# Optimization experiments

Measured on AMD Instinct MI355X. Metric: run time of the kernel, lower is better.

Reference implementation:

```python
import jax, jax.numpy as jnp
import numpy as np

B, F, HU, HC = 8192, 100, 128, 512


def _lin(key, din, dout, bias=True, scale=0.02):
    k1, k2 = jax.random.split(key)
    w = jax.random.normal(k1, (din, dout), jnp.float32) * scale
    if bias:
        b = jax.random.normal(k2, (dout,), jnp.float32) * scale
        return w, b
    return (w,)


def setup_inputs() -> dict:
    key = jax.random.key(0)
    ks = jax.random.split(key, 24)
    d = {}
    d['feature_list'] = jax.random.normal(ks[0], (B, F), jnp.float32)
    d['is_treat'] = jax.random.uniform(ks[1], (B,), jnp.float32)
    d['emb'] = jax.random.normal(ks[2], (F, HU), jnp.float32) * 0.02
    d['t_w'], d['t_b'] = _lin(ks[3], 1, HU)
    d['qw'], d['qb'] = _lin(ks[4], HU, HU)
    d['kw'], d['kb'] = _lin(ks[5], HU, HU)
    d['vw'], d['vb'] = _lin(ks[6], HU, HU)
    (d['a1w'],) = _lin(ks[7], HU, HU, bias=False)
    d['a2w'], d['a2b'] = _lin(ks[8], HU, HU)
    (d['a3w'],) = _lin(ks[9], HU, 1, bias=False)
    d['c1w'], d['c1b'] = _lin(ks[10], F * HU, HC)
    d['c2w'], d['c2b'] = _lin(ks[11], HC, HC)
    d['c3w'], d['c3b'] = _lin(ks[12], HC, HC // 2)
    d['c4w'], d['c4b'] = _lin(ks[13], HC // 2, HC // 4)
    d['c5w'], d['c5b'] = _lin(ks[14], HC // 4, HC // 8)
    d['clw'], d['clb'] = _lin(ks[15], HC // 8, 1)
    d['ctw'], d['ctb'] = _lin(ks[16], HC // 8, 1)
    d['u1w'], d['u1b'] = _lin(ks[17], HU, HU)
    d['u2w'], d['u2b'] = _lin(ks[18], HU, HU // 2)
    d['u3w'], d['u3b'] = _lin(ks[19], HU // 2, HU // 4)
    d['u4w'], d['u4b'] = _lin(ks[20], HU // 4, HU // 8)
    d['tlw'], d['tlb'] = _lin(ks[21], HU // 8, 1)
    d['utw'], d['utb'] = _lin(ks[22], HU // 8, 1)
    return d


def reference(feature_list, is_treat, emb, t_w, t_b, qw, qb, kw, kb, vw, vb,
              a1w, a2w, a2b, a3w, c1w, c1b, c2w, c2b, c3w, c3b, c4w, c4b,
              c5w, c5b, clw, clb, ctw, ctb, u1w, u1b, u2w, u2b, u3w, u3b,
              u4w, u4b, tlw, tlb, utw, utb):
    elu = jax.nn.elu
    sig = jax.nn.sigmoid
    b, f = feature_list.shape
    h = emb.shape[1]
    # per-feature embedding: [B, F, H]
    x_rep = feature_list[:, :, None] * emb[None, :, :]
    # normalize over the feature axis (dim=1), as in torch.linalg.norm(dim=1)
    nx = x_rep / jnp.linalg.norm(x_rep, axis=1, keepdims=True)
    # self-attention with sigmoid-then-softmax scores
    Q = nx @ qw + qb
    K = nx @ kw + kb
    V = nx @ vw + vb
    scores = jnp.einsum('bfh,bgh->bfg', Q, K) / (h ** 0.5)
    attn_w = jax.nn.softmax(sig(scores), axis=-1)
    xx = jnp.einsum('bfg,bgh->bfh', attn_w, V).reshape(b, f * h)
    # control net tower
    c = elu(xx @ c1w + c1b)
    c = elu(c @ c2w + c2b)
    c = elu(c @ c3w + c3b)
    c = elu(c @ c4w + c4b)
    c = elu(c @ c5w + c5b)  # is_self=True
    c_logit = c @ clw + clb
    c_tau = c @ ctw + ctb
    c_prob = sig(c_logit)
    # treatment representation: Linear(1, hu) on ones -> [B, H]
    t_rep = jnp.ones((b, 1), feature_list.dtype) @ t_w.reshape(1, h) + t_b
    # interaction attention (vectorized over features)
    att = jax.nn.relu(sig(t_rep @ a1w)[:, None, :] + sig(x_rep @ a2w + a2b))
    att = (att @ a3w)[..., 0]  # [B, F]
    attn = jax.nn.softmax(att, axis=1)
    xt = jnp.einsum('bf,bfh->bh', attn, x_rep)
    # uplift net tower
    u = elu(xt @ u1w + u1b)
    u = elu(u @ u2w + u2b)
    u = elu(u @ u3w + u3b)
    u = elu(u @ u4w + u4b)  # is_self=True
    t_logit = u @ tlw + tlb
    u_tau = u @ utw + utb
    t_prob = sig(t_logit)
    return (c_logit, c_prob, c_tau, t_logit, t_prob, u_tau)
```

## Files before the change

### kernel.cpp

```cpp
#include <hip/hip_runtime.h>
#include <hip/hip_bf16.h>

typedef __bf16 bf16;
typedef __bf16 bf16x8 __attribute__((ext_vector_type(8)));
typedef __bf16 bf16x4 __attribute__((ext_vector_type(4)));
typedef float f32x4 __attribute__((ext_vector_type(4)));
typedef unsigned u32x4 __attribute__((ext_vector_type(4)));

#define DEVI static __device__ __forceinline__

DEVI float sigmoidf_(float x){ return 1.0f/(1.0f+__expf(-x)); }
DEVI float eluf_(float x){ return x>0.f ? x : (__expf(x)-1.f); }
DEVI f32x4 mfma16(bf16x8 a, bf16x8 b, f32x4 c){ return __builtin_amdgcn_mfma_f32_16x16x32_bf16(a,b,c,0,0,0); }
DEVI f32x4 mfma8(long a, long b, f32x4 c){ return __builtin_amdgcn_mfma_f32_16x16x32_fp8_fp8(a,b,c,0,0,0); }
DEVI unsigned pack2_(float a, float b){
    union { bf16 v[2]; unsigned u; } t; t.v[0]=(bf16)a; t.v[1]=(bf16)b; return t.u;
}
DEVI unsigned long long pack4_(float a, float b, float c, float d){
    union { bf16 v[4]; unsigned long long u; } t;
    t.v[0]=(bf16)a; t.v[1]=(bf16)b; t.v[2]=(bf16)c; t.v[3]=(bf16)d; return t.u;
}
DEVI unsigned cvtfp8x4_(float a, float b, float c, float d){
    int v = __builtin_amdgcn_cvt_pk_fp8_f32(a, b, 0, false);
    v = __builtin_amdgcn_cvt_pk_fp8_f32(c, d, v, true);
    return (unsigned)v;
}
DEVI bf16x8 ldb64x2(const bf16* p0, const bf16* p1){
    union { bf16x8 v8; bf16x4 v4[2]; } u;
    u.v4[0] = *(const bf16x4*)p0;
    u.v4[1] = *(const bf16x4*)p1;
    return u.v8;
}

#define B_ 8192
#define F_ 100
#define FP 112
#define H_ 128
#define KC_ 12800
#define SPLIT_ 4
#define FP8SC 16.0f

#define SWZ(r,bc) ((bc) ^ (((r)&7)<<4))

DEVI void dotrans_(float (*t)[33], const float* in, bf16* out, int R, int C, int bx, int by, int tid){
    int c0 = bx*32, r0 = by*32;
    int tc = tid & 31, tr = tid >> 5;
    #pragma unroll
    for (int i=0;i<4;i++){
        int r = tr + i*8;
        t[r][tc] = in[(size_t)(r0+r)*C + c0 + tc];
    }
    __syncthreads();
    #pragma unroll
    for (int i=0;i<4;i++){
        int ro = tr + i*8;
        out[(size_t)(c0+ro)*R + r0 + tc] = (bf16)t[tc][ro];
    }
}

__global__ void k_prep_all(const float* __restrict__ qw, const float* __restrict__ qb,
                           const float* __restrict__ kw, const float* __restrict__ kb,
                           const float* __restrict__ tw, const float* __restrict__ tb,
                           const float* __restrict__ a1w, const float* __restrict__ vw,
                           const float* __restrict__ a2w, const float* __restrict__ c2w,
                           const float* __restrict__ c3w,
                           bf16* __restrict__ mextT, float* __restrict__ sigt, float* __restrict__ cconst,
                           bf16* __restrict__ wvT, bf16* __restrict__ wa2t,
                           bf16* __restrict__ c2wt, bf16* __restrict__ c3wt){
    __shared__ float t[32][33];
    const float rsc = 0.08838834764831845f;
    int blk = blockIdx.x, tid = threadIdx.x;
    if (blk < 9){
        #pragma unroll 1
        for (int e=0; e<8; ++e){
            int idx = e*256 + tid;
            int n = blk*16 + (idx>>7), h = idx&127;
            float acc = 0.f;
            if (n < 128){
                for (int d=0; d<128; ++d) acc += qw[h*128+d]*kw[n*128+d];
            } else if (n == 128){
                for (int d=0; d<128; ++d) acc += qw[h*128+d]*kb[d];
            } else if (n == 129){
                for (int d=0; d<128; ++d) acc += kw[h*128+d]*qb[d];
            }
            mextT[n*128+h] = (bf16)(acc*rsc);
        }
    } else if (blk == 9){
        if (tid < 128){
            float acc = 0.f;
            for (int h=0; h<128; ++h) acc += (tw[h]+tb[h]) * a1w[h*128+tid];
            sigt[tid] = sigmoidf_(acc);
        } else if (tid == 128){
            float acc = 0.f;
            for (int d=0; d<128; ++d) acc += qb[d]*kb[d];
            cconst[0] = acc*rsc;
        }
    } else if (blk < 26){
        int i = blk-10; dotrans_(t, vw, wvT, 128,128, i&3, i>>2, tid);
    } else if (blk < 42){
        int i = blk-26; dotrans_(t, a2w, wa2t, 128,128, i&3, i>>2, tid);
    } else if (blk < 298){
        int i = blk-42; dotrans_(t, c2w, c2wt, 512,512, i&15, i>>4, tid);
    } else {
        int i = blk-298; dotrans_(t, c3w, c3wt, 512,256, i&7, i>>3, tid);
    }
}

DEVI int kappa_(int k){
    int f = k>>7, h = k&127;
    if (f < 96)
        return (((f>>4)<<3) | (h>>4))*256 + ((f&15)>>2)*64 + (h&15)*4 + (f&3);
    else
        return 12288 + (h>>4)*64 + (h&15)*4 + (f&3);
}
__global__ void k_tc_kappa8(const float* __restrict__ in, unsigned char* __restrict__ out){
    __shared__ float t[32][33];
    const int C = 512;
    int c0 = blockIdx.x*32, r0 = blockIdx.y*32;
    int tc = threadIdx.x & 31, tr = threadIdx.x >> 5;
    #pragma unroll
    for (int i=0;i<4;i++){
        int r = tr + i*8;
        t[r][tc] = in[(size_t)(r0+r)*C + c0 + tc];
    }
    __syncthreads();
    #pragma unroll
    for (int i=0;i<4;i++){
        int ro = tr + i*8;
        float x = t[tc][ro]*FP8SC;
        int v = __builtin_amdgcn_cvt_pk_fp8_f32(x, x, 0, false);
        out[(size_t)(c0+ro)*KC_ + kappa_(r0+tc)] = (unsigned char)v;
    }
}

__global__ __launch_bounds__(256,2) void k_gatt(
    const float* __restrict__ feat, const float* __restrict__ emb,
    const bf16* __restrict__ wa2t, const float* __restrict__ a2b,
    const float* __restrict__ a3w, const float* __restrict__ sigt,
    float* __restrict__ attg)
{
    __shared__ bf16 sAt[128][72];
    __shared__ bf16 sBt[128][72];
    __shared__ float sRed[2][128];
    int tid=threadIdx.x, w=tid>>6, lane=tid&63, l15=lane&15, l4=lane>>4;
    int m0 = blockIdx.x*128;
    int wr = w>>1, wc = w&1;
    f32x4 acc[4][4];
    #pragma unroll
    for(int mi=0;mi<4;mi++)
        #pragma unroll
        for(int ni=0;ni<4;ni++) acc[mi][ni] = (f32x4){0.f,0.f,0.f,0.f};

    #pragma unroll 1
    for (int k0=0; k0<128; k0+=64){
        __syncthreads();
        #pragma unroll
        for (int t4=0; t4<4; t4++){
            int t = tid + t4*256;
            int row=t>>3, col=(t&7)*8;
            int gr = m0+row;
            int bb = gr/112, ff = gr - bb*112;
            bf16x8 o;
            if (ff < F_){
                float fv = feat[(size_t)bb*F_ + ff];
                const float* ep = emb + ff*H_ + k0 + col;
                f32x4 e0 = *(const f32x4*)ep;
                f32x4 e1 = *(const f32x4*)(ep+4);
                o[0]=(bf16)(fv*e0[0]); o[1]=(bf16)(fv*e0[1]); o[2]=(bf16)(fv*e0[2]); o[3]=(bf16)(fv*e0[3]);
                o[4]=(bf16)(fv*e1[0]); o[5]=(bf16)(fv*e1[1]); o[6]=(bf16)(fv*e1[2]); o[7]=(bf16)(fv*e1[3]);
            } else {
                #pragma unroll
                for (int e=0;e<8;e++) o[e]=(bf16)0.f;
            }
            *(bf16x8*)&sAt[row][col] = o;
            *(bf16x8*)&sBt[row][col] = *(const bf16x8*)(wa2t + row*H_ + k0 + col);
        }
        __syncthreads();
        #pragma unroll
        for(int ks=0;ks<2;ks++){
            bf16x8 af[4], bfr[4];
            #pragma unroll
            for(int mi=0;mi<4;mi++) af[mi] = *(const bf16x8*)&sAt[wr*64+mi*16+l15][ks*32+l4*8];
            #pragma unroll
            for(int ni=0;ni<4;ni++) bfr[ni] = *(const bf16x8*)&sBt[wc*64+ni*16+l15][ks*32+l4*8];
            #pragma unroll
            for(int mi=0;mi<4;mi++)
                #pragma unroll
                for(int ni=0;ni<4;ni++)
                    acc[mi][ni] = mfma16(af[mi], bfr[ni], acc[mi][ni]);
        }
    }
    float sg[4], ab[4], a3[4];
    #pragma unroll
    for (int ni=0;ni<4;ni++){
        int n = wc*64 + ni*16 + l15;
        sg[ni]=sigt[n]; ab[ni]=a2b[n]; a3[ni]=a3w[n];
    }
    #pragma unroll
    for (int mi=0;mi<4;mi++){
        float sj[4] = {0.f,0.f,0.f,0.f};
        #pragma unroll
        for (int ni=0;ni<4;ni++){
            #pragma unroll
            for (int j=0;j<4;j++){
                float u = sigmoidf_(acc[mi][ni][j] + ab[ni]);
                float t = sg[ni] + u;
                t = t>0.f ? t : 0.f;
                sj[j] += t*a3[ni];
            }
        }
        #pragma unroll
        for (int j=0;j<4;j++){
            float v = sj[j];
            #pragma unroll
            for (int m=1;m<16;m<<=1) v += __shfl_xor(v,m,16);
            sj[j]=v;
        }
        if (l15==0){
            #pragma unroll
            for (int j=0;j<4;j++) sRed[wc][wr*64+mi*16+l4*4+j] = sj[j];
        }
    }
    __syncthreads();
    if (tid < 128) attg[(size_t)m0 + tid] = sRed[0][tid] + sRed[1][tid];
}

__global__ __launch_bounds__(512,2) void k_attn2(
    const float* __restrict__ feat, const float* __restrict__ emb,
    const bf16* __restrict__ mextT, const bf16* __restrict__ wvT,
    const float* __restrict__ vb, const float* __restrict__ cconst,
    const float* __restrict__ attg,
    unsigned char* __restrict__ xxb, bf16* __restrict__ xtb)
{
    __shared__ char L[81792];
    char* Lm = L;
    char* Ln = L + 33280;
    float* sFeat  = (float*)(L+61952);
    float* sAw    = (float*)(L+62400);
    float* normP  = (float*)(L+62848);
    float* xtP    = (float*)(L+66944);
    float* sNorm  = (float*)(L+80384);
    float* sAlpha = (float*)(L+80896);
    float* sBeta  = (float*)(L+81344);

    int b = blockIdx.x;
    int tid = threadIdx.x, w = tid>>6, lane = tid&63;
    int l15 = lane&15, l4 = lane>>4;
    bf16 (*sP)[72] = (bf16(*)[72])(L + 61952 + w*2304);

    bf16x8 awv[4];
    #pragma unroll
    for (int kc=0;kc<4;kc++)
        awv[kc] = *(const bf16x8*)(wvT + (w*16+l15)*H_ + kc*32 + l4*8);
    float vbr[4];
    #pragma unroll
    for (int j=0;j<4;j++) vbr[j] = vb[w*16+l4*4+j];

    #pragma unroll 2
    for (int v = tid; v < 130*16; v += 512){
        int n = v >> 4, cg = (v & 15) * 8;
        *(u32x4*)(Lm + n*256 + SWZ(n, cg*2)) = *(const u32x4*)(mextT + n*128 + cg);
    }
    if (tid < FP) sFeat[tid] = (tid<F_) ? feat[(size_t)b*F_+tid] : 0.f;
    if (w==0){
        const float* ag = attg + (size_t)b*FP;
        float a0 = (lane<F_)? ag[lane] : -1e30f;
        float a1 = (lane+64<F_)? ag[lane+64] : -1e30f;
        float m = fmaxf(a0,a1);
        #pragma unroll
        for(int s=1;s<64;s<<=1) m = fmaxf(m, __shfl_xor(m,s,64));
        float e0 = (lane<F_)? __expf(a0-m):0.f;
        float e1 = (lane+64<F_)? __expf(a1-m):0.f;
        float s = e0+e1;
        #pragma unroll
        for(int t=1;t<64;t<<=1) s += __shfl_xor(s,t,64);
        float inv = 1.f/s;
        if (lane<FP) sAw[lane] = e0*inv;
        if (lane+64<FP) sAw[lane+64] = e1*inv;
    }
    __syncthreads();

    int hp = (tid&63)*2, gg = tid>>6;
    {
        float fa0=0.f, fa1=0.f;
        #pragma unroll 4
        for (int it=0; it<13; ++it){
            int f = gg + 8*it;
            if (f < F_){
                float2 e2 = *(const float2*)(emb + f*H_ + hp);
                float v0 = sFeat[f]*e2.x, v1 = sFeat[f]*e2.y;
                fa0 += v0*v0; fa1 += v1*v1;
            }
        }
        *(float2*)(normP + gg*128 + hp) = make_float2(fa0, fa1);
    }
    __syncthreads();
    if (tid < 128){
        float s = 0.f;
        #pragma unroll
        for (int g2=0; g2<8; ++g2) s += normP[g2*128 + tid];
        sNorm[tid] = sqrtf(s);
    }
    __syncthreads();

    {
        float rn0 = __builtin_amdgcn_rcpf(sNorm[hp]);
        float rn1 = __builtin_amdgcn_rcpf(sNorm[hp+1]);
        #pragma unroll 4
        for (int it=0; it<13; ++it){
            int f = gg + 8*it;
            if (f < F_){
                float2 e2 = *(const float2*)(emb + f*H_ + hp);
                *(unsigned*)(Ln + f*256 + SWZ(f, hp*2)) = pack2_(sFeat[f]*e2.x*rn0, sFeat[f]*e2.y*rn1);
            }
        }
        for (int z=tid; z<768; z+=512){
            int f = 100 + (z>>6), hz = (z&63)*2;
            *(unsigned*)(Ln + f*256 + SWZ(f, hz*2)) = 0u;
        }
    }
    __syncthreads();

    int mt = w;

    if (mt < 7){
        int nrow = 128 + (l15&1);
        bf16x8 bfr8[4];
        #pragma unroll
        for (int kc=0;kc<4;kc++)
            bfr8[kc] = *(const bf16x8*)(Lm + nrow*256 + SWZ(nrow, (kc*32+l4*8)*2));
        f32x4 acc = {0.f,0.f,0.f,0.f};
        #pragma unroll
        for (int kc=0;kc<4;kc++){
            bf16x8 a = *(const bf16x8*)(Ln + (mt*16+l15)*256 + SWZ(mt*16+l15, (kc*32+l4*8)*2));
            acc = mfma16(a, bfr8[kc], acc);
        }
        if (l15==0){
            #pragma unroll
            for (int j=0;j<4;j++) sAlpha[mt*16+l4*4+j] = acc[j];
        }
        if (l15==1){
            #pragma unroll
            for (int j=0;j<4;j++) sBeta[mt*16+l4*4+j] = acc[j];
        }
    }
    {
        int g4 = tid>>7, h = tid&127;
        float acc=0.f;
        #pragma unroll 5
        for (int it=0; it<25; ++it){
            int f = g4 + 4*it;
            acc += sAw[f] * (float)*(const bf16*)(Ln + f*256 + SWZ(f, h*2));
        }
        xtP[g4*128+h] = acc;
    }
    __syncthreads();
    if (tid < 128)
        xtb[(size_t)b*H_+tid] = (bf16)((xtP[tid]+xtP[128+tid]+xtP[256+tid]+xtP[384+tid]) * sNorm[tid]);
    __syncthreads();

    const float cc = cconst[0];
    unsigned uexB[3][2];
    float inv_[4];
    if (mt < 7){
        bf16x8 afxi[4];
        #pragma unroll
        for (int kc=0;kc<4;kc++)
            afxi[kc] = *(const bf16x8*)(Ln + (mt*16+l15)*256 + SWZ(mt*16+l15, (kc*32+l4*8)*2));
        f32x4 sc[7];
        #pragma unroll
        for (int gt=0; gt<7; gt++) sc[gt] = (f32x4){0.f,0.f,0.f,0.f};
        #pragma unroll 1
        for (int p=0; p<2; p++){
            #pragma unroll 2
            for (int nt4=0; nt4<4; nt4++){
                int nt = p*4 + nt4;
                bf16x8 bw[4];
                #pragma unroll
                for (int kc=0;kc<4;kc++)
                    bw[kc] = *(const bf16x8*)(Lm + (nt*16+l15)*256 + SWZ(nt*16+l15, (kc*32+l4*8)*2));
                f32x4 d = {0.f,0.f,0.f,0.f};
                #pragma unroll
                for (int kc=0;kc<4;kc++) d = mfma16(afxi[kc], bw[kc], d);
                #pragma unroll
                for (int j=0;j<4;j++) sP[l4*4+j][nt4*16+l15] = (bf16)d[j];
            }
            bf16x8 afs0 = *(const bf16x8*)&sP[l15][l4*8];
            bf16x8 afs1 = *(const bf16x8*)&sP[l15][32+l4*8];
            #pragma unroll
            for (int gt=0; gt<7; gt++){
                int r = gt*16+l15;
                bf16x8 b0 = *(const bf16x8*)(Ln + r*256 + SWZ(r, (p*64 + l4*8)*2));
                bf16x8 b1 = *(const bf16x8*)(Ln + r*256 + SWZ(r, (p*64 + 32 + l4*8)*2));
                sc[gt] = mfma16(afs0, b0, sc[gt]);
                sc[gt] = mfma16(afs1, b1, sc[gt]);
            }
        }
        float aj[4];
        #pragma unroll
        for (int j=0;j<4;j++) aj[j] = sAlpha[mt*16+l4*4+j];
        float rs[4] = {0.f,0.f,0.f,0.f};
        #pragma unroll
        for (int gt=0; gt<7; gt++){
            float bg = sBeta[gt*16+l15];
            int g = gt*16+l15;
            float e[4];
            #pragma unroll
            for (int j=0;j<4;j++){
                float val = sc[gt][j] + aj[j] + bg + cc;
                e[j] = (g<F_) ? __expf(sigmoidf_(val)) : 0.f;
                rs[j] += e[j];
            }
            if (gt < 4){
                #pragma unroll
                for (int j=0;j<4;j++) sP[l4*4+j][gt*16+l15] = (bf16)e[j];
            } else {
                uexB[gt-4][0] = pack2_(e[0],e[1]);
                uexB[gt-4][1] = pack2_(e[2],e[3]);
            }
        }
        #pragma unroll
        for (int j=0;j<4;j++){
            float v = rs[j];
            #pragma unroll
            for (int m2=1;m2<16;m2<<=1) v += __shfl_xor(v,m2,16);
            inv_[j] = 1.f/v;
        }
    }

    unsigned vpk[7][2];
    {
        #pragma unroll
        for (int gt=0; gt<7; gt++){
            f32x4 acc = {0.f,0.f,0.f,0.f};
            #pragma unroll
            for (int kc=0;kc<4;kc++){
                int r = gt*16+l15;
                bf16x8 bfr = *(const bf16x8*)(Ln + r*256 + SWZ(r, (kc*32+l4*8)*2));
                acc = mfma16(awv[kc], bfr, acc);
            }
            vpk[gt][0] = pack2_(acc[0]+vbr[0], acc[1]+vbr[1]);
            vpk[gt][1] = pack2_(acc[2]+vbr[2], acc[3]+vbr[3]);
        }
    }
    __syncthreads();

    union UP { unsigned u; bf16 v[2]; };
    {
        int ht = w;
        #pragma unroll
        for (int gt=0; gt<7; gt++){
            UP u0, u1;
            u0.u = vpk[gt][0]; u1.u = vpk[gt][1];
            int r0 = ht*16+l4*4;
            *(bf16*)(Ln + (r0  )*224 + SWZ(r0,   (gt*16+l15)*2)) = u0.v[0];
            *(bf16*)(Ln + (r0+1)*224 + SWZ(r0+1, (gt*16+l15)*2)) = u0.v[1];
            *(bf16*)(Ln + (r0+2)*224 + SWZ(r0+2, (gt*16+l15)*2)) = u1.v[0];
            *(bf16*)(Ln + (r0+3)*224 + SWZ(r0+3, (gt*16+l15)*2)) = u1.v[1];
        }
    }
    __syncthreads();

    if (mt < 7){
        bf16x8 ap0 = *(const bf16x8*)&sP[l15][l4*8];
        bf16x8 ap1 = *(const bf16x8*)&sP[l15][32+l4*8];
        f32x4 acc8[8];
        #pragma unroll
        for (int ht=0;ht<8;ht++) acc8[ht] = (f32x4){0.f,0.f,0.f,0.f};
        #pragma unroll
        for (int ht=0; ht<8; ht++){
            int r = ht*16+l15;
            int c0 = l4*8, c1 = 32+l4*8;
            acc8[ht] = mfma16(ap0, ldb64x2((const bf16*)(Ln + r*224 + SWZ(r, c0*2)),
                                           (const bf16*)(Ln + r*224 + SWZ(r, (c0+4)*2))), acc8[ht]);
            acc8[ht] = mfma16(ap1, ldb64x2((const bf16*)(Ln + r*224 + SWZ(r, c1*2)),
                                           (const bf16*)(Ln + r*224 + SWZ(r, (c1+4)*2))), acc8[ht]);
        }
        #pragma unroll
        for (int gt=4; gt<7; gt++){
            #pragma unroll
            for (int j2=0; j2<2; j2++){
                UP u; u.u = uexB[gt-4][j2];
                sP[l4*4+j2*2  ][(gt-4)*16+l15] = u.v[0];
                sP[l4*4+j2*2+1][(gt-4)*16+l15] = u.v[1];
            }
        }
        #pragma unroll
        for (int j=0;j<4;j++) sP[l4*4+j][48+l15] = (bf16)0.f;
        bf16x8 ap2 = *(const bf16x8*)&sP[l15][l4*8];
        bf16x8 ap3 = *(const bf16x8*)&sP[l15][32+l4*8];
        #pragma unroll
        for (int ht=0; ht<8; ht++){
            int r = ht*16+l15;
            int c2 = 64+l4*8;
            int c3 = 96+l4*8;  if (c3 >= 112) c3 = 96;
            acc8[ht] = mfma16(ap2, ldb64x2((const bf16*)(Ln + r*224 + SWZ(r, c2*2)),
                                           (const bf16*)(Ln + r*224 + SWZ(r, (c2+4)*2))), acc8[ht]);
            acc8[ht] = mfma16(ap3, ldb64x2((const bf16*)(Ln + r*224 + SWZ(r, c3*2)),
                                           (const bf16*)(Ln + r*224 + SWZ(r, (c3+4)*2))), acc8[ht]);
        }
        float fs[4];
        #pragma unroll
        for (int j=0;j<4;j++) fs[j] = inv_[j]*FP8SC;
        #pragma unroll
        for (int ht=0; ht<8; ht++){
            unsigned u = cvtfp8x4_(acc8[ht][0]*fs[0], acc8[ht][1]*fs[1], acc8[ht][2]*fs[2], acc8[ht][3]*fs[3]);
            if (mt < 6){
                *(unsigned*)(xxb + (size_t)b*KC_ + (mt*8+ht)*256 + lane*4) = u;
            } else if (l4 == 0){
                *(unsigned*)(xxb + (size_t)b*KC_ + 12288 + ht*64 + l15*4) = u;
            }
        }
    }
}

__global__ __launch_bounds__(256,2) void k_gemm_fp8(const unsigned char* __restrict__ A,
        const unsigned char* __restrict__ Bt, float* __restrict__ part, int M, int N, int K, int KS)
{
    __shared__ unsigned char sA[128][72];
    __shared__ unsigned char sB[128][72];
    int tid=threadIdx.x, w=tid>>6, lane=tid&63, l15=lane&15, l4=lane>>4;
    int m0 = blockIdx.y*128, n0 = blockIdx.x*128;
    int kbeg = blockIdx.z*KS, kend = kbeg + KS;
    int wr = w>>1, wc = w&1;
    f32x4 acc[4][4];
    #pragma unroll
    for(int mi=0;mi<4;mi++)
        #pragma unroll
        for(int ni=0;ni<4;ni++) acc[mi][ni] = (f32x4){0.f,0.f,0.f,0.f};

    for (int k0=kbeg; k0<kend; k0+=64){
        __syncthreads();
        #pragma unroll
        for (int t2=0;t2<2;t2++){
            int t = tid + t2*256;
            int row=t>>2, col=(t&3)*16;
            *(u32x4*)&sA[row][col] = *(const u32x4*)(A + (size_t)(m0+row)*K + k0 + col);
            *(u32x4*)&sB[row][col] = *(const u32x4*)(Bt + (size_t)(n0+row)*K + k0 + col);
        }
        __syncthreads();
        #pragma unroll
        for(int ks=0;ks<2;ks++){
            long af[4], bfr[4];
            #pragma unroll
            for(int mi=0;mi<4;mi++) af[mi] = *(const long*)&sA[wr*64+mi*16+l15][ks*32+l4*8];
            #pragma unroll
            for(int ni=0;ni<4;ni++) bfr[ni] = *(const long*)&sB[wc*64+ni*16+l15][ks*32+l4*8];
            #pragma unroll
            for(int mi=0;mi<4;mi++)
                #pragma unroll
                for(int ni=0;ni<4;ni++)
                    acc[mi][ni] = mfma8(af[mi], bfr[ni], acc[mi][ni]);
        }
    }
    float* pz = part + (size_t)blockIdx.z*M*N;
    #pragma unroll
    for(int mi=0;mi<4;mi++)
        #pragma unroll
        for(int ni=0;ni<4;ni++){
            int col = n0 + wc*64 + ni*16 + l15;
            #pragma unroll
            for(int j=0;j<4;j++){
                int row = m0 + wr*64 + mi*16 + l4*4 + j;
                pz[(size_t)row*N + col] = acc[mi][ni][j];
            }
        }
}

__global__ void k_c1fin(const float* __restrict__ part, const float* __restrict__ bias,
                        bf16* __restrict__ out){
    const size_t MN = (size_t)B_*512;
    size_t e0 = ((size_t)blockIdx.x*256 + threadIdx.x)*4;
    f32x4 s = *(const f32x4*)(part + e0);
    s += *(const f32x4*)(part + MN + e0);
    s += *(const f32x4*)(part + 2*MN + e0);
    s += *(const f32x4*)(part + 3*MN + e0);
    f32x4 bb = *(const f32x4*)(bias + (e0 & 511));
    const float ds = 1.0f/(FP8SC*FP8SC);
    unsigned long long u = pack4_(eluf_(s[0]*ds+bb[0]), eluf_(s[1]*ds+bb[1]),
                                  eluf_(s[2]*ds+bb[2]), eluf_(s[3]*ds+bb[3]));
    *(unsigned long long*)(out + e0) = u;
}

template<int BN, bool ELU>
__global__ __launch_bounds__(256,2) void k_gemm(const bf16* __restrict__ A, const bf16* __restrict__ Bt,
        const float* __restrict__ bias, bf16* __restrict__ out, int M, int N, int K)
{
    __shared__ bf16 sAt[128][72];
    __shared__ bf16 sBt[BN][72];
    int tid=threadIdx.x, w=tid>>6, lane=tid&63, l15=lane&15, l4=lane>>4;
    int m0 = blockIdx.y*128, n0 = blockIdx.x*BN;
    constexpr int MI = (BN==128)?4:2;
    constexpr int NI = (BN==128)?4:BN/16;
    int wr = (BN==128)? (w>>1) : w;
    int wc = (BN==128)? (w&1) : 0;
    f32x4 acc[MI][NI];
    #pragma unroll
    for(int mi=0;mi<MI;mi++)
        #pragma unroll
        for(int ni=0;ni<NI;ni++) acc[mi][ni] = (f32x4){0.f,0.f,0.f,0.f};

    for (int k0=0; k0<K; k0+=64){
        __syncthreads();
        for (int t=tid; t<128*8; t+=256){
            int row=t>>3, col=(t&7)*8;
            *(bf16x8*)&sAt[row][col] = *(const bf16x8*)(A + (size_t)(m0+row)*K + k0 + col);
        }
        for (int t=tid; t<BN*8; t+=256){
            int row=t>>3, col=(t&7)*8;
            *(bf16x8*)&sBt[row][col] = *(const bf16x8*)(Bt + (size_t)(n0+row)*K + k0 + col);
        }
        __syncthreads();
        #pragma unroll
        for(int ks=0;ks<2;ks++){
            bf16x8 af[MI], bfr[NI];
            #pragma unroll
            for(int mi=0;mi<MI;mi++) af[mi] = *(const bf16x8*)&sAt[wr*(MI*16)+mi*16+l15][ks*32+l4*8];
            #pragma unroll
            for(int ni=0;ni<NI;ni++) bfr[ni] = *(const bf16x8*)&sBt[wc*64+ni*16+l15][ks*32+l4*8];
            #pragma unroll
            for(int mi=0;mi<MI;mi++)
                #pragma unroll
                for(int ni=0;ni<NI;ni++)
                    acc[mi][ni] = mfma16(af[mi], bfr[ni], acc[mi][ni]);
        }
    }
    #pragma unroll
    for(int mi=0;mi<MI;mi++)
        #pragma unroll
        for(int ni=0;ni<NI;ni++){
            int col = n0 + wc*64 + ni*16 + l15;
            float bc = bias[col];
            #pragma unroll
            for(int j=0;j<4;j++){
                int row = m0 + wr*(MI*16) + mi*16 + l4*4 + j;
                float v = acc[mi][ni][j] + bc;
                if (ELU) v = eluf_(v);
                out[(size_t)row*N + col] = (bf16)v;
            }
        }
}

__global__ __launch_bounds__(256,2) void k_ctail(const bf16* __restrict__ c3o,
    const float* __restrict__ c4w, const float* __restrict__ c4b,
    const float* __restrict__ c5w, const float* __restrict__ c5b,
    const float* __restrict__ clw, const float* __restrict__ clb,
    const float* __restrict__ ctw, const float* __restrict__ ctb, float* __restrict__ outp)
{
    __shared__ float sA[32][260];
    __shared__ float sB[32][132];
    __shared__ float sC[32][68];
    int tid = threadIdx.x; int r0 = blockIdx.x*32;
    for (int v=tid; v<32*64; v+=256){
        int r=v>>6, c=(v&63)*4;
        bf16x4 x = *(const bf16x4*)(c3o + (size_t)(r0+r)*256 + c);
        sA[r][c]=(float)x[0]; sA[r][c+1]=(float)x[1]; sA[r][c+2]=(float)x[2]; sA[r][c+3]=(float)x[3];
    }
    __syncthreads();
    {
        int j = tid&127, rb = tid>>7;
        float acc[16];
        #pragma unroll
        for (int i=0;i<16;i++) acc[i]=c4b[j];
        #pragma unroll 4
        for (int h=0;h<256;h++){
            float wv = c4w[h*128+j];
            #pragma unroll
            for (int i=0;i<16;i++) acc[i] += sA[2*i+rb][h]*wv;
        }
        #pragma unroll
        for (int i=0;i<16;i++) sB[2*i+rb][j] = eluf_(acc[i]);
    }
    __syncthreads();
    {
        int j = tid&63, rb = tid>>6;
        float acc[8];
        #pragma unroll
        for (int i=0;i<8;i++) acc[i]=c5b[j];
        #pragma unroll 4
        for (int h=0;h<128;h++){
            float wv = c5w[h*64+j];
            #pragma unroll
            for (int i=0;i<8;i++) acc[i] += sB[4*i+rb][h]*wv;
        }
        #pragma unroll
        for (int i=0;i<8;i++) sC[4*i+rb][j] = eluf_(acc[i]);
    }
    __syncthreads();
    if (tid < 32){
        float r1 = clb[0], r2 = ctb[0];
        #pragma unroll 8
        for (int k=0;k<64;k++){ float v = sC[tid][k]; r1 += v*clw[k]; r2 += v*ctw[k]; }
        int row = r0 + tid;
        outp[row] = r1;
        outp[B_ + row] = sigmoidf_(r1);
        outp[(size_t)2*B_ + row] = r2;
    }
}

__global__ __launch_bounds__(256,2) void k_utower(const bf16* __restrict__ xtb,
    const float* __restrict__ u1w, const float* __restrict__ u1b,
    const float* __restrict__ u2w, const float* __restrict__ u2b,
    const float* __restrict__ u3w, const float* __restrict__ u3b,
    const float* __restrict__ u4w, const float* __restrict__ u4b,
    const float* __restrict__ tlw, const float* __restrict__ tlb,
    const float* __restrict__ utw, const float* __restrict__ utb, float* __restrict__ outp)
{
    __shared__ float sA[32][132];
    __shared__ float sB[32][132];
    __shared__ float sC[32][68];
    __shared__ float sD[32][36];
    __shared__ float sE[32][20];
    int tid = threadIdx.x; int r0 = blockIdx.x*32;
    for (int v=tid; v<32*32; v+=256){
        int r=v>>5, c=(v&31)*4;
        bf16x4 x = *(const bf16x4*)(xtb + (size_t)(r0+r)*128 + c);
        sA[r][c]=(float)x[0]; sA[r][c+1]=(float)x[1]; sA[r][c+2]=(float)x[2]; sA[r][c+3]=(float)x[3];
    }
    __syncthreads();
    {
        int j = tid&127, rb = tid>>7;
        float acc[16];
        #pragma unroll
        for (int i=0;i<16;i++) acc[i]=u1b[j];
        #pragma unroll 4
        for (int h=0;h<128;h++){
            float wv = u1w[h*128+j];
            #pragma unroll
            for (int i=0;i<16;i++) acc[i] += sA[2*i+rb][h]*wv;
        }
        #pragma unroll
        for (int i=0;i<16;i++) sB[2*i+rb][j] = eluf_(acc[i]);
    }
    __syncthreads();
    {
        int j = tid&63, rb = tid>>6;
        float acc[8];
        #pragma unroll
        for (int i=0;i<8;i++) acc[i]=u2b[j];
        #pragma unroll 4
        for (int h=0;h<128;h++){
            float wv = u2w[h*64+j];
            #pragma unroll
            for (int i=0;i<8;i++) acc[i] += sB[4*i+rb][h]*wv;
        }
        #pragma unroll
        for (int i=0;i<8;i++) sC[4*i+rb][j] = eluf_(acc[i]);
    }
    __syncthreads();
    {
        int j = tid&31, rb = tid>>5;
        float acc[4];
        #pragma unroll
        for (int i=0;i<4;i++) acc[i]=u3b[j];
        #pragma unroll 4
        for (int h=0;h<64;h++){
            float wv = u3w[h*32+j];
            #pragma unroll
            for (int i=0;i<4;i++) acc[i] += sC[8*i+rb][h]*wv;
        }
        #pragma unroll
        for (int i=0;i<4;i++) sD[8*i+rb][j] = eluf_(acc[i]);
    }
    __syncthreads();
    {
        int j = tid&15, rb = tid>>4;
        float acc[2];
        acc[0]=u4b[j]; acc[1]=u4b[j];
        #pragma unroll 4
        for (int h=0;h<32;h++){
            float wv = u4w[h*16+j];
            acc[0] += sD[rb][h]*wv;
            acc[1] += sD[16+rb][h]*wv;
        }
        sE[rb][j] = eluf_(acc[0]);
        sE[16+rb][j] = eluf_(acc[1]);
    }
    __syncthreads();
    if (tid < 32){
        float r1 = tlb[0], r2 = utb[0];
        #pragma unroll
        for (int k=0;k<16;k++){ float v = sE[tid][k]; r1 += v*tlw[k]; r2 += v*utw[k]; }
        int row = r0 + tid;
        outp[(size_t)3*B_ + row] = r1;
        outp[(size_t)4*B_ + row] = sigmoidf_(r1);
        outp[(size_t)5*B_ + row] = r2;
    }
}

extern "C" void kernel_launch(void* const* d_in, const int* in_sizes, int n_in,
                              void* d_out, int out_size, void* d_ws, size_t ws_size,
                              hipStream_t stream) {
    const float* feat=(const float*)d_in[0];
    const float* emb =(const float*)d_in[2];
    const float* t_w =(const float*)d_in[3]; const float* t_b=(const float*)d_in[4];
    const float* qw  =(const float*)d_in[5]; const float* qb =(const float*)d_in[6];
    const float* kw  =(const float*)d_in[7]; const float* kb =(const float*)d_in[8];
    const float* vw  =(const float*)d_in[9]; const float* vb =(const float*)d_in[10];
    const float* a1w =(const float*)d_in[11];
    const float* a2w =(const float*)d_in[12]; const float* a2b=(const float*)d_in[13];
    const float* a3w =(const float*)d_in[14];
    const float* c1w =(const float*)d_in[15]; const float* c1b=(const float*)d_in[16];
    const float* c2w =(const float*)d_in[17]; const float* c2b=(const float*)d_in[18];
    const float* c3w =(const float*)d_in[19]; const float* c3b=(const float*)d_in[20];
    const float* c4w =(const float*)d_in[21]; const float* c4b=(const float*)d_in[22];
    const float* c5w =(const float*)d_in[23]; const float* c5b=(const float*)d_in[24];
    const float* clw =(const float*)d_in[25]; const float* clb=(const float*)d_in[26];
    const float* ctw =(const float*)d_in[27]; const float* ctb=(const float*)d_in[28];
    const float* u1w =(const float*)d_in[29]; const float* u1b=(const float*)d_in[30];
    const float* u2w =(const float*)d_in[31]; const float* u2b=(const float*)d_in[32];
    const float* u3w =(const float*)d_in[33]; const float* u3b=(const float*)d_in[34];
    const float* u4w =(const float*)d_in[35]; const float* u4b=(const float*)d_in[36];
    const float* tlw =(const float*)d_in[37]; const float* tlb=(const float*)d_in[38];
    const float* utw =(const float*)d_in[39]; const float* utb=(const float*)d_in[40];
    float* outp = (float*)d_out;

    char* ws = (char*)d_ws;
    size_t off = 0;
    auto alloc = [&](size_t bytes)->char*{ char* p = ws + off; off += (bytes + 255) & ~(size_t)255; return p; };
    unsigned char* xxb = (unsigned char*)alloc((size_t)B_*KC_);
    float* part  = (float*)alloc((size_t)SPLIT_*B_*512*4);
    float* attg  = (float*)alloc((size_t)B_*FP*4);
    bf16* xtb    = (bf16*)alloc((size_t)B_*128*2);
    bf16* cbuf1  = (bf16*)alloc((size_t)B_*512*2);
    bf16* mextT  = (bf16*)alloc(144*128*2);
    bf16* wvT    = (bf16*)alloc(128*128*2);
    bf16* wa2t   = (bf16*)alloc(128*128*2);
    unsigned char* c1wtk8 = (unsigned char*)alloc((size_t)512*KC_);
    bf16* c2wt   = (bf16*)alloc((size_t)512*512*2);
    bf16* c3wt   = (bf16*)alloc((size_t)512*256*2);
    float* sigt  = (float*)alloc(128*4);
    float* cconst= (float*)alloc(4);
    bf16* cbuf2 = (bf16*)(xxb);
    bf16* cbuf3 = (bf16*)(xxb + (16u<<20));
    (void)ws_size; (void)in_sizes; (void)n_in; (void)out_size;

    k_prep_all<<<426,256,0,stream>>>(qw,qb,kw,kb,t_w,t_b,a1w, vw, a2w, c2w, c3w,
                                     mextT, sigt, cconst, wvT, wa2t, c2wt, c3wt);
    k_tc_kappa8<<<dim3(16,400),256,0,stream>>>(c1w, c1wtk8);

    k_gatt<<<7168,256,0,stream>>>(feat, emb, wa2t, a2b, a3w, sigt, attg);

    k_attn2<<<B_,512,0,stream>>>(feat,emb,mextT,wvT,vb,cconst,attg, xxb, xtb);

    k_utower<<<256,256,0,stream>>>(xtb,u1w,u1b,u2w,u2b,u3w,u3b,u4w,u4b,tlw,tlb,utw,utb,outp);

    k_gemm_fp8<<<dim3(4,64,SPLIT_),256,0,stream>>>(xxb, c1wtk8, part, B_,512,KC_, KC_/SPLIT_);
    k_c1fin<<<4096,256,0,stream>>>(part, c1b, cbuf1);

    k_gemm<128,true><<<dim3(4,64),256,0,stream>>>(cbuf1, c2wt, c2b, cbuf2, B_,512,512);
    k_gemm<128,true><<<dim3(2,64),256,0,stream>>>(cbuf2, c3wt, c3b, cbuf3, B_,256,512);
    k_ctail<<<256,256,0,stream>>>(cbuf3,c4w,c4b,c5w,c5b,clw,clb,ctw,ctb,outp);
}
```

Measured before the change: 728.2 us.

## Reduce c1 split-K, single-pass gatt staging, transposed MFMA layouts in attn2

Halves the split-K factor for the big fp8 c1 GEMM, which cuts partial-sum traffic and the reduction work in the finalize kernel, at the cost of fewer blocks and longer K loops per block. The gatt kernel now stages the full 128-wide K dimension in shared memory in one pass instead of two, removing a barrier round. The attention kernel swaps MFMA operand order so outputs land row-contiguous, which allows packed 64-bit shared-memory stores and drops scalar bf16 scatter and shuffle reductions. The V tile is written into the freed Lm buffer with full 16-byte reads, and the softmax inverse is passed through shared memory.

```diff
diff --git a/kernel.cpp b/kernel.cpp
--- a/kernel.cpp
+++ b/kernel.cpp
@@ -25,19 +25,13 @@
     v = __builtin_amdgcn_cvt_pk_fp8_f32(c, d, v, true);
     return (unsigned)v;
 }
-DEVI bf16x8 ldb64x2(const bf16* p0, const bf16* p1){
-    union { bf16x8 v8; bf16x4 v4[2]; } u;
-    u.v4[0] = *(const bf16x4*)p0;
-    u.v4[1] = *(const bf16x4*)p1;
-    return u.v8;
-}
 
 #define B_ 8192
 #define F_ 100
 #define FP 112
 #define H_ 128
 #define KC_ 12800
-#define SPLIT_ 4
+#define SPLIT_ 2
 #define FP8SC 16.0f
 
 #define SWZ(r,bc) ((bc) ^ (((r)&7)<<4))
@@ -139,8 +133,8 @@
     const float* __restrict__ a3w, const float* __restrict__ sigt,
     float* __restrict__ attg)
 {
-    __shared__ bf16 sAt[128][72];
-    __shared__ bf16 sBt[128][72];
+    __shared__ bf16 sAt[128][136];
+    __shared__ bf16 sBt[128][136];
     __shared__ float sRed[2][128];
     int tid=threadIdx.x, w=tid>>6, lane=tid&63, l15=lane&15, l4=lane>>4;
     int m0 = blockIdx.x*128;
@@ -151,44 +145,40 @@
         #pragma unroll
         for(int ni=0;ni<4;ni++) acc[mi][ni] = (f32x4){0.f,0.f,0.f,0.f};
 
-    #pragma unroll 1
-    for (int k0=0; k0<128; k0+=64){
-        __syncthreads();
-        #pragma unroll
-        for (int t4=0; t4<4; t4++){
-            int t = tid + t4*256;
-            int row=t>>3, col=(t&7)*8;
-            int gr = m0+row;
-            int bb = gr/112, ff = gr - bb*112;
-            bf16x8 o;
-            if (ff < F_){
-                float fv = feat[(size_t)bb*F_ + ff];
-                const float* ep = emb + ff*H_ + k0 + col;
-                f32x4 e0 = *(const f32x4*)ep;
-                f32x4 e1 = *(const f32x4*)(ep+4);
-                o[0]=(bf16)(fv*e0[0]); o[1]=(bf16)(fv*e0[1]); o[2]=(bf16)(fv*e0[2]); o[3]=(bf16)(fv*e0[3]);
-                o[4]=(bf16)(fv*e1[0]); o[5]=(bf16)(fv*e1[1]); o[6]=(bf16)(fv*e1[2]); o[7]=(bf16)(fv*e1[3]);
-            } else {
-                #pragma unroll
-                for (int e=0;e<8;e++) o[e]=(bf16)0.f;
-            }
-            *(bf16x8*)&sAt[row][col] = o;
-            *(bf16x8*)&sBt[row][col] = *(const bf16x8*)(wa2t + row*H_ + k0 + col);
-        }
-        __syncthreads();
-        #pragma unroll
-        for(int ks=0;ks<2;ks++){
-            bf16x8 af[4], bfr[4];
-            #pragma unroll
-            for(int mi=0;mi<4;mi++) af[mi] = *(const bf16x8*)&sAt[wr*64+mi*16+l15][ks*32+l4*8];
-            #pragma unroll
-            for(int ni=0;ni<4;ni++) bfr[ni] = *(const bf16x8*)&sBt[wc*64+ni*16+l15][ks*32+l4*8];
-            #pragma unroll
-            for(int mi=0;mi<4;mi++)
-                #pragma unroll
-                for(int ni=0;ni<4;ni++)
-                    acc[mi][ni] = mfma16(af[mi], bfr[ni], acc[mi][ni]);
-        }
+    #pragma unroll 2
+    for (int t8=0; t8<8; t8++){
+        int v = tid + t8*256;
+        int row = v>>4, colg = (v&15)*8;
+        int gr = m0+row;
+        int bb = gr/112, ff = gr - bb*112;
+        bf16x8 o;
+        if (ff < F_){
+            float fv = feat[(size_t)bb*F_ + ff];
+            const float* ep = emb + ff*H_ + colg;
+            f32x4 e0 = *(const f32x4*)ep;
+            f32x4 e1 = *(const f32x4*)(ep+4);
+            o[0]=(bf16)(fv*e0[0]); o[1]=(bf16)(fv*e0[1]); o[2]=(bf16)(fv*e0[2]); o[3]=(bf16)(fv*e0[3]);
+            o[4]=(bf16)(fv*e1[0]); o[5]=(bf16)(fv*e1[1]); o[6]=(bf16)(fv*e1[2]); o[7]=(bf16)(fv*e1[3]);
+        } else {
+            #pragma unroll
+            for (int e=0;e<8;e++) o[e]=(bf16)0.f;
+        }
+        *(bf16x8*)&sAt[row][colg] = o;
+        *(bf16x8*)&sBt[row][colg] = *(const bf16x8*)(wa2t + row*H_ + colg);
+    }
+    __syncthreads();
+    #pragma unroll
+    for(int ks=0;ks<4;ks++){
+        bf16x8 af[4], bfr[4];
+        #pragma unroll
+        for(int mi=0;mi<4;mi++) af[mi] = *(const bf16x8*)&sAt[wr*64+mi*16+l15][ks*32+l4*8];
+        #pragma unroll
+        for(int ni=0;ni<4;ni++) bfr[ni] = *(const bf16x8*)&sBt[wc*64+ni*16+l15][ks*32+l4*8];
+        #pragma unroll
+        for(int mi=0;mi<4;mi++)
+            #pragma unroll
+            for(int ni=0;ni<4;ni++)
+                acc[mi][ni] = mfma16(af[mi], bfr[ni], acc[mi][ni]);
     }
     float sg[4], ab[4], a3[4];
     #pragma unroll
@@ -234,30 +224,29 @@
 {
     __shared__ char L[81792];
     char* Lm = L;
-    char* Ln = L + 33280;
-    float* sFeat  = (float*)(L+61952);
-    float* sAw    = (float*)(L+62400);
-    float* normP  = (float*)(L+62848);
-    float* xtP    = (float*)(L+66944);
-    float* sNorm  = (float*)(L+80384);
-    float* sAlpha = (float*)(L+80896);
-    float* sBeta  = (float*)(L+81344);
+    char* Ln = L + 32768;
+    float* sFeat  = (float*)(L+61440);
+    float* sAw    = (float*)(L+61888);
+    float* normP  = (float*)(L+62336);
+    float* xtP    = (float*)(L+66432);
+    float* sNorm  = (float*)(L+79872);
+    float* sAlpha = (float*)(L+80384);
+    float* sBeta  = (float*)(L+80832);
+    float* sInv   = (float*)(L+81280);
 
     int b = blockIdx.x;
     int tid = threadIdx.x, w = tid>>6, lane = tid&63;
     int l15 = lane&15, l4 = lane>>4;
-    bf16 (*sP)[72] = (bf16(*)[72])(L + 61952 + w*2304);
+    bf16 (*sP)[72] = (bf16(*)[72])(L + 61440 + w*2304);
 
     bf16x8 awv[4];
     #pragma unroll
     for (int kc=0;kc<4;kc++)
         awv[kc] = *(const bf16x8*)(wvT + (w*16+l15)*H_ + kc*32 + l4*8);
-    float vbr[4];
-    #pragma unroll
-    for (int j=0;j<4;j++) vbr[j] = vb[w*16+l4*4+j];
+    float vbr = vb[w*16+l15];
 
     #pragma unroll 2
-    for (int v = tid; v < 130*16; v += 512){
+    for (int v = tid; v < 128*16; v += 512){
         int n = v >> 4, cg = (v & 15) * 8;
         *(u32x4*)(Lm + n*256 + SWZ(n, cg*2)) = *(const u32x4*)(mextT + n*128 + cg);
     }
@@ -324,11 +313,10 @@
     int mt = w;
 
     if (mt < 7){
-        int nrow = 128 + (l15&1);
         bf16x8 bfr8[4];
         #pragma unroll
         for (int kc=0;kc<4;kc++)
-            bfr8[kc] = *(const bf16x8*)(Lm + nrow*256 + SWZ(nrow, (kc*32+l4*8)*2));
+            bfr8[kc] = *(const bf16x8*)(mextT + (128+(l15&1))*H_ + kc*32 + l4*8);
         f32x4 acc = {0.f,0.f,0.f,0.f};
         #pragma unroll
         for (int kc=0;kc<4;kc++){
@@ -360,8 +348,7 @@
     __syncthreads();
 
     const float cc = cconst[0];
-    unsigned uexB[3][2];
-    float inv_[4];
+    unsigned long long uexB[3];
     if (mt < 7){
         bf16x8 afxi[4];
         #pragma unroll
@@ -381,9 +368,8 @@
                     bw[kc] = *(const bf16x8*)(Lm + (nt*16+l15)*256 + SWZ(nt*16+l15, (kc*32+l4*8)*2));
                 f32x4 d = {0.f,0.f,0.f,0.f};
                 #pragma unroll
-                for (int kc=0;kc<4;kc++) d = mfma16(afxi[kc], bw[kc], d);
-                #pragma unroll
-                for (int j=0;j<4;j++) sP[l4*4+j][nt4*16+l15] = (bf16)d[j];
+                for (int kc=0;kc<4;kc++) d = mfma16(bw[kc], afxi[kc], d);
+                *(unsigned long long*)(&sP[l15][nt4*16 + l4*4]) = pack4_(d[0],d[1],d[2],d[3]);
             }
             bf16x8 afs0 = *(const bf16x8*)&sP[l15][l4*8];
             bf16x8 afs1 = *(const bf16x8*)&sP[l15][32+l4*8];
@@ -392,72 +378,52 @@
                 int r = gt*16+l15;
                 bf16x8 b0 = *(const bf16x8*)(Ln + r*256 + SWZ(r, (p*64 + l4*8)*2));
                 bf16x8 b1 = *(const bf16x8*)(Ln + r*256 + SWZ(r, (p*64 + 32 + l4*8)*2));
-                sc[gt] = mfma16(afs0, b0, sc[gt]);
-                sc[gt] = mfma16(afs1, b1, sc[gt]);
-            }
-        }
-        float aj[4];
-        #pragma unroll
-        for (int j=0;j<4;j++) aj[j] = sAlpha[mt*16+l4*4+j];
-        float rs[4] = {0.f,0.f,0.f,0.f};
+                sc[gt] = mfma16(b0, afs0, sc[gt]);
+                sc[gt] = mfma16(b1, afs1, sc[gt]);
+            }
+        }
+        float aj = sAlpha[mt*16+l15];
+        float rs = 0.f;
         #pragma unroll
         for (int gt=0; gt<7; gt++){
-            float bg = sBeta[gt*16+l15];
-            int g = gt*16+l15;
+            f32x4 bt4 = *(const f32x4*)&sBeta[gt*16+l4*4];
             float e[4];
             #pragma unroll
             for (int j=0;j<4;j++){
-                float val = sc[gt][j] + aj[j] + bg + cc;
+                int g = gt*16 + l4*4 + j;
+                float val = sc[gt][j] + aj + bt4[j] + cc;
                 e[j] = (g<F_) ? __expf(sigmoidf_(val)) : 0.f;
-                rs[j] += e[j];
-            }
-            if (gt < 4){
-                #pragma unroll
-                for (int j=0;j<4;j++) sP[l4*4+j][gt*16+l15] = (bf16)e[j];
-            } else {
-                uexB[gt-4][0] = pack2_(e[0],e[1]);
-                uexB[gt-4][1] = pack2_(e[2],e[3]);
-            }
-        }
-        #pragma unroll
-        for (int j=0;j<4;j++){
-            float v = rs[j];
-            #pragma unroll
-            for (int m2=1;m2<16;m2<<=1) v += __shfl_xor(v,m2,16);
-            inv_[j] = 1.f/v;
-        }
-    }
-
-    unsigned vpk[7][2];
-    {
-        #pragma unroll
-        for (int gt=0; gt<7; gt++){
-            f32x4 acc = {0.f,0.f,0.f,0.f};
-            #pragma unroll
-            for (int kc=0;kc<4;kc++){
-                int r = gt*16+l15;
-                bf16x8 bfr = *(const bf16x8*)(Ln + r*256 + SWZ(r, (kc*32+l4*8)*2));
-                acc = mfma16(awv[kc], bfr, acc);
-            }
-            vpk[gt][0] = pack2_(acc[0]+vbr[0], acc[1]+vbr[1]);
-            vpk[gt][1] = pack2_(acc[2]+vbr[2], acc[3]+vbr[3]);
-        }
-    }
-    __syncthreads();
-
-    union UP { unsigned u; bf16 v[2]; };
-    {
-        int ht = w;
-        #pragma unroll
-        for (int gt=0; gt<7; gt++){
-            UP u0, u1;
-            u0.u = vpk[gt][0]; u1.u = vpk[gt][1];
-            int r0 = ht*16+l4*4;
-            *(bf16*)(Ln + (r0  )*224 + SWZ(r0,   (gt*16+l15)*2)) = u0.v[0];
-            *(bf16*)(Ln + (r0+1)*224 + SWZ(r0+1, (gt*16+l15)*2)) = u0.v[1];
-            *(bf16*)(Ln + (r0+2)*224 + SWZ(r0+2, (gt*16+l15)*2)) = u1.v[0];
-            *(bf16*)(Ln + (r0+3)*224 + SWZ(r0+3, (gt*16+l15)*2)) = u1.v[1];
-        }
+                rs += e[j];
+            }
+            if (gt < 4)
+                *(unsigned long long*)(&sP[l15][gt*16 + l4*4]) = pack4_(e[0],e[1],e[2],e[3]);
+            else
+                uexB[gt-4] = pack4_(e[0],e[1],e[2],e[3]);
+        }
+        rs += __shfl_xor(rs, 16, 64);
+        rs += __shfl_xor(rs, 32, 64);
+        if (l4 == 0) sInv[w*16 + l15] = 1.f/rs;
+    }
+
+    unsigned long long vpku[7];
+    #pragma unroll
+    for (int gt=0; gt<7; gt++){
+        f32x4 acc = {0.f,0.f,0.f,0.f};
+        #pragma unroll
+        for (int kc=0;kc<4;kc++){
+            int r = gt*16+l15;
+            bf16x8 a = *(const bf16x8*)(Ln + r*256 + SWZ(r, (kc*32+l4*8)*2));
+            acc = mfma16(a, awv[kc], acc);
+        }
+        vpku[gt] = pack4_(acc[0]+vbr, acc[1]+vbr, acc[2]+vbr, acc[3]+vbr);
+    }
+    __syncthreads();
+
+    {
+        int hrow = w*16 + l15;
+        #pragma unroll
+        for (int gt=0; gt<7; gt++)
+            *(unsigned long long*)(Lm + hrow*256 + SWZ(hrow, gt*32 + l4*8)) = vpku[gt];
     }
     __syncthreads();
 
@@ -470,23 +436,15 @@
         #pragma unroll
         for (int ht=0; ht<8; ht++){
             int r = ht*16+l15;
-            int c0 = l4*8, c1 = 32+l4*8;
-            acc8[ht] = mfma16(ap0, ldb64x2((const bf16*)(Ln + r*224 + SWZ(r, c0*2)),
-                                           (const bf16*)(Ln + r*224 + SWZ(r, (c0+4)*2))), acc8[ht]);
-            acc8[ht] = mfma16(ap1, ldb64x2((const bf16*)(Ln + r*224 + SWZ(r, c1*2)),
-                                           (const bf16*)(Ln + r*224 + SWZ(r, (c1+4)*2))), acc8[ht]);
-        }
-        #pragma unroll
-        for (int gt=4; gt<7; gt++){
-            #pragma unroll
-            for (int j2=0; j2<2; j2++){
-                UP u; u.u = uexB[gt-4][j2];
-                sP[l4*4+j2*2  ][(gt-4)*16+l15] = u.v[0];
-                sP[l4*4+j2*2+1][(gt-4)*16+l15] = u.v[1];
-            }
-        }
-        #pragma unroll
-        for (int j=0;j<4;j++) sP[l4*4+j][48+l15] = (bf16)0.f;
+            bf16x8 bv0 = *(const bf16x8*)(Lm + r*256 + SWZ(r, (l4*8)*2));
+            bf16x8 bv1 = *(const bf16x8*)(Lm + r*256 + SWZ(r, (32+l4*8)*2));
+            acc8[ht] = mfma16(ap0, bv0, acc8[ht]);
+            acc8[ht] = mfma16(ap1, bv1, acc8[ht]);
+        }
+        #pragma unroll
+        for (int gt=4; gt<7; gt++)
+            *(unsigned long long*)(&sP[l15][(gt-4)*16 + l4*4]) = uexB[gt-4];
+        *(unsigned long long*)(&sP[l15][48 + l4*4]) = 0ull;
         bf16x8 ap2 = *(const bf16x8*)&sP[l15][l4*8];
         bf16x8 ap3 = *(const bf16x8*)&sP[l15][32+l4*8];
         #pragma unroll
@@ -494,14 +452,14 @@
             int r = ht*16+l15;
             int c2 = 64+l4*8;
             int c3 = 96+l4*8;  if (c3 >= 112) c3 = 96;
-            acc8[ht] = mfma16(ap2, ldb64x2((const bf16*)(Ln + r*224 + SWZ(r, c2*2)),
-                                           (const bf16*)(Ln + r*224 + SWZ(r, (c2+4)*2))), acc8[ht]);
-            acc8[ht] = mfma16(ap3, ldb64x2((const bf16*)(Ln + r*224 + SWZ(r, c3*2)),
-                                           (const bf16*)(Ln + r*224 + SWZ(r, (c3+4)*2))), acc8[ht]);
+            bf16x8 bv2 = *(const bf16x8*)(Lm + r*256 + SWZ(r, c2*2));
+            bf16x8 bv3 = *(const bf16x8*)(Lm + r*256 + SWZ(r, c3*2));
+            acc8[ht] = mfma16(ap2, bv2, acc8[ht]);
+            acc8[ht] = mfma16(ap3, bv3, acc8[ht]);
         }
         float fs[4];
         #pragma unroll
-        for (int j=0;j<4;j++) fs[j] = inv_[j]*FP8SC;
+        for (int j=0;j<4;j++) fs[j] = sInv[w*16 + l4*4 + j] * FP8SC;
         #pragma unroll
         for (int ht=0; ht<8; ht++){
             unsigned u = cvtfp8x4_(acc8[ht][0]*fs[0], acc8[ht][1]*fs[1], acc8[ht][2]*fs[2], acc8[ht][3]*fs[3]);
@@ -573,8 +531,6 @@
     size_t e0 = ((size_t)blockIdx.x*256 + threadIdx.x)*4;
     f32x4 s = *(const f32x4*)(part + e0);
     s += *(const f32x4*)(part + MN + e0);
-    s += *(const f32x4*)(part + 2*MN + e0);
-    s += *(const f32x4*)(part + 3*MN + e0);
     f32x4 bb = *(const f32x4*)(bias + (e0 & 511));
     const float ds = 1.0f/(FP8SC*FP8SC);
     unsigned long long u = pack4_(eluf_(s[0]*ds+bb[0]), eluf_(s[1]*ds+bb[1]),
@@ -765,16 +721,15 @@
     __syncthreads();
     {
         int j = tid&15, rb = tid>>4;
-        float acc[2];
-        acc[0]=u4b[j]; acc[1]=u4b[j];
+        float acc0=u4b[j], acc1=u4b[j];
         #pragma unroll 4
         for (int h=0;h<32;h++){
             float wv = u4w[h*16+j];
-            acc[0] += sD[rb][h]*wv;
-            acc[1] += sD[16+rb][h]*wv;
-        }
-        sE[rb][j] = eluf_(acc[0]);
-        sE[16+rb][j] = eluf_(acc[1]);
+            acc0 += sD[rb][h]*wv;
+            acc1 += sD[16+rb][h]*wv;
+        }
+        sE[rb][j] = eluf_(acc0);
+        sE[16+rb][j] = eluf_(acc1);
     }
     __syncthreads();
     if (tid < 32){
```

New measurement: 729.3 us. About the same (+0.2%).
